# Kernel tuning notes

Measured on AMD Instinct MI355X. Metric: run time of the kernel, lower is better.

Reference implementation:

```python
import jax, jax.numpy as jnp
import numpy as np

N, T, CIN, H, L, NC = 64, 150, 150, 1024, 3, 60
EPS = 1e-5


def setup_inputs() -> dict:
    key = jax.random.key(0)
    ks = jax.random.split(key, 12)
    s = 0.05
    return {
        "x": jax.random.normal(ks[0], (N, T, CIN), jnp.float32),
        "bn_gamma": jnp.ones((CIN,), jnp.float32),
        "bn_beta": jnp.zeros((CIN,), jnp.float32),
        "w_ih0": jax.random.normal(ks[1], (2, 3 * H, CIN), jnp.float32) * s,
        "w_hh0": jax.random.normal(ks[2], (2, 3 * H, H), jnp.float32) * s,
        "b_ih0": jax.random.normal(ks[3], (2, 3 * H), jnp.float32) * s,
        "b_hh0": jax.random.normal(ks[4], (2, 3 * H), jnp.float32) * s,
        "w_ih": jax.random.normal(ks[5], (L - 1, 2, 3 * H, 2 * H), jnp.float32) * s,
        "w_hh": jax.random.normal(ks[6], (L - 1, 2, 3 * H, H), jnp.float32) * s,
        "b_ih": jax.random.normal(ks[7], (L - 1, 2, 3 * H), jnp.float32) * s,
        "b_hh": jax.random.normal(ks[8], (L - 1, 2, 3 * H), jnp.float32) * s,
        "fc_w": jax.random.normal(ks[9], (NC, 2 * H), jnp.float32) * s,
        "fc_b": jax.random.normal(ks[10], (NC,), jnp.float32) * s,
    }


def _bigru_layer(x, w_ih, w_hh, b_ih, b_hh):
    # x: [T, N, I]. Faithful to the source's per-timestep loop: BOTH directions
    # scan forward in time (the 'reverse' direction never sees a reversed seq,
    # since the original feeds length-1 slices while carrying hidden state).
    # Precompute input projections for the whole sequence: [T, 2, N, 3H]
    gi = jnp.einsum('tni,dgi->tdng', x, w_ih) + b_ih[None, :, None, :]

    def step(h, gi_t):
        # h: [2, N, H], gi_t: [2, N, 3H]
        gh = jnp.einsum('dnh,dgh->dng', h, w_hh) + b_hh[:, None, :]
        r = jax.nn.sigmoid(gi_t[..., :H] + gh[..., :H])
        z = jax.nn.sigmoid(gi_t[..., H:2 * H] + gh[..., H:2 * H])
        n = jnp.tanh(gi_t[..., 2 * H:] + r * gh[..., 2 * H:])
        h_new = (1.0 - z) * n + z * h
        out = jnp.concatenate([h_new[0], h_new[1]], axis=-1)  # [N, 2H]
        return h_new, out

    h0 = jnp.zeros((2, x.shape[1], H), x.dtype)
    _, outs = jax.lax.scan(step, h0, gi)
    return outs  # [T, N, 2H]


def reference(x, bn_gamma, bn_beta, w_ih0, w_hh0, b_ih0, b_hh0,
              w_ih, w_hh, b_ih, b_hh, fc_w, fc_b):
    # BatchNorm1d over channels, train mode: batch stats over (N, T), biased var.
    mean = x.mean(axis=(0, 1))
    var = x.var(axis=(0, 1))
    xn = (x - mean) * jax.lax.rsqrt(var + EPS) * bn_gamma + bn_beta

    h = jnp.transpose(xn, (1, 0, 2))  # [T, N, CIN]
    h = _bigru_layer(h, w_ih0, w_hh0, b_ih0, b_hh0)
    for l in range(L - 1):  # small fixed layer loop
        h = _bigru_layer(h, w_ih[l], w_hh[l], b_ih[l], b_hh[l])

    # seq_len == T for every sample, so the gathered hidden is the last step.
    last = h[-1]  # [N, 2H]
    return last @ fc_w.T + fc_b  # [N, num_class]
```

## Files before the change

### kernel.cpp

```cpp
#include <hip/hip_runtime.h>
#include <math.h>

#define NB   64
#define TT   150
#define CIN  150
#define HH   1024
#define G3   3072
#define NCOL 6144
#define KP0  160
#define RT   9600
#define NC   60
#define NSLOT 151
#define SLOT_STRIDE 66560

using bf16x8 = __attribute__((ext_vector_type(8))) __bf16;
using f32x4  = __attribute__((ext_vector_type(4))) float;

static __device__ __forceinline__ unsigned short f2bf(float f){
  unsigned int x = __builtin_bit_cast(unsigned int, f);
  x += 0x7fffu + ((x >> 16) & 1u);
  return (unsigned short)(x >> 16);
}
static __device__ __forceinline__ float bf2f(unsigned short u){
  unsigned int x = ((unsigned int)u) << 16;
  return __builtin_bit_cast(float, x);
}
static __device__ __forceinline__ float sigmoidf(float x){
  return 1.0f / (1.0f + expf(-x));
}

static __device__ __forceinline__ void gload16(const void* g, void* l){
  __builtin_amdgcn_global_load_lds(
      (const __attribute__((address_space(1))) void*)g,
      (__attribute__((address_space(3))) void*)l, 16, 0, 0);
}

__global__ void bn_stats(const float* __restrict__ x, const float* __restrict__ gamma,
                         const float* __restrict__ beta, float* __restrict__ ss){
  const int c = blockIdx.x;
  float s = 0.f, s2 = 0.f;
  for (int i = threadIdx.x; i < RT; i += 256){
    float v = x[(size_t)i * CIN + c];
    s += v; s2 += v * v;
  }
  __shared__ float sh1[256], sh2[256];
  sh1[threadIdx.x] = s; sh2[threadIdx.x] = s2;
  __syncthreads();
  for (int st = 128; st > 0; st >>= 1){
    if ((int)threadIdx.x < st){
      sh1[threadIdx.x] += sh1[threadIdx.x + st];
      sh2[threadIdx.x] += sh2[threadIdx.x + st];
    }
    __syncthreads();
  }
  if (threadIdx.x == 0){
    float mean = sh1[0] * (1.f / RT);
    float var  = sh2[0] * (1.f / RT) - mean * mean;
    float sc   = rsqrtf(var + 1e-5f) * gamma[c];
    ss[c]       = sc;
    ss[CIN + c] = beta[c] - mean * sc;
  }
}

__global__ void bn_apply(const float* __restrict__ x, const float* __restrict__ ss,
                         unsigned short* __restrict__ xn){
  int idx = blockIdx.x * 256 + threadIdx.x;
  if (idx >= RT * KP0) return;
  int r = idx / KP0, c = idx - r * KP0;
  int t = r >> 6, n = r & 63;
  float v = 0.f;
  if (c < CIN) v = x[((size_t)n * TT + t) * CIN + c] * ss[c] + ss[CIN + c];
  xn[idx] = f2bf(v);
}

__global__ void cast_bf(const float* __restrict__ s, unsigned short* __restrict__ d, int n){
  for (int i = blockIdx.x * 256 + threadIdx.x; i < n; i += gridDim.x * 256)
    d[i] = f2bf(s[i]);
}

__global__ void cast_pad_w0(const float* __restrict__ w, unsigned short* __restrict__ d){
  int idx = blockIdx.x * 256 + threadIdx.x;
  if (idx >= NCOL * KP0) return;
  int row = idx / KP0, c = idx - row * KP0;
  d[idx] = (c < CIN) ? f2bf(w[(size_t)row * CIN + c]) : (unsigned short)0;
}

__global__ void zero16(uint4* p, int n){
  int i = blockIdx.x * 256 + threadIdx.x;
  if (i < n) p[i] = make_uint4(0u, 0u, 0u, 0u);
}

__global__ void guard_k(float* out){ out[0] = -12345.0f; }

__global__ __launch_bounds__(256) void gemm_tile(
    const unsigned short* __restrict__ A, const unsigned short* __restrict__ B,
    const float* __restrict__ bias, unsigned short* __restrict__ C, int K)
{
  const int r0 = blockIdx.x * 128;
  const int c0 = blockIdx.y * 128;
  const int tid = threadIdx.x;
  const int wid = tid >> 6;
  const int l   = tid & 63;
  const int lr  = l & 15;
  const int lk  = (l >> 4) * 8;
  const int wm  = wid >> 1;
  const int wn  = wid & 1;

  __shared__ unsigned short As[128 * 32];
  __shared__ unsigned short Bs[128 * 32];

  const int c1   = wid * 64 + l;
  const int rowS = c1 >> 2;
  const int ccS  = c1 & 3;

  f32x4 acc[4][4];
#pragma unroll
  for (int i = 0; i < 4; ++i)
#pragma unroll
    for (int j = 0; j < 4; ++j) acc[i][j] = f32x4{0,0,0,0};

  const unsigned short* Ag0 = A + (size_t)(r0 + rowS) * K + ccS * 8;
  const unsigned short* Ag1 = A + (size_t)(r0 + 64 + rowS) * K + ccS * 8;
  const unsigned short* Bg0 = B + (size_t)(c0 + rowS) * K + ccS * 8;
  const unsigned short* Bg1 = B + (size_t)(c0 + 64 + rowS) * K + ccS * 8;
  unsigned short* As0 = As + wid * 512;
  unsigned short* As1 = As + 2048 + wid * 512;
  unsigned short* Bs0 = Bs + wid * 512;
  unsigned short* Bs1 = Bs + 2048 + wid * 512;

  for (int k0 = 0; k0 < K; k0 += 32){
    gload16(Ag0 + k0, As0);
    gload16(Ag1 + k0, As1);
    gload16(Bg0 + k0, Bs0);
    gload16(Bg1 + k0, Bs1);
    __syncthreads();

    bf16x8 af[4], bfr[4];
#pragma unroll
    for (int mt = 0; mt < 4; ++mt)
      af[mt] = *(const bf16x8*)(As + (wm * 64 + mt * 16 + lr) * 32 + lk);
#pragma unroll
    for (int nt = 0; nt < 4; ++nt)
      bfr[nt] = *(const bf16x8*)(Bs + (wn * 64 + nt * 16 + lr) * 32 + lk);
#pragma unroll
    for (int mt = 0; mt < 4; ++mt)
#pragma unroll
      for (int nt = 0; nt < 4; ++nt)
        acc[mt][nt] = __builtin_amdgcn_mfma_f32_16x16x32_bf16(af[mt], bfr[nt], acc[mt][nt], 0, 0, 0);
    __syncthreads();
  }

  const int rb = (l >> 4) * 4;
#pragma unroll
  for (int mt = 0; mt < 4; ++mt){
#pragma unroll
    for (int nt = 0; nt < 4; ++nt){
      const int col = c0 + wn * 64 + nt * 16 + lr;
      const float bv = bias[col];
#pragma unroll
      for (int reg = 0; reg < 4; ++reg){
        const int row = r0 + wm * 64 + mt * 16 + rb + reg;
        C[(size_t)row * NCOL + col] = f2bf(acc[mt][nt][reg] + bv);
      }
    }
  }
}

__global__ __launch_bounds__(512, 1) void gru_layer(
    const unsigned short* __restrict__ whh,
    const float* __restrict__ bhh,
    const unsigned short* __restrict__ gi,
    unsigned short* __restrict__ outb,
    float* __restrict__ hfinal,
    unsigned short* __restrict__ hbig,
    int* __restrict__ flags, int wout)
{
  const int d  = blockIdx.x >> 6;
  const int jt = blockIdx.x & 63;
  const int j0 = jt * 16;
  const int tid = threadIdx.x;
  const int w  = tid >> 6;
  const int wq = w & 3;
  const int kh = w >> 2;
  const int l  = tid & 63;
  const int lr = l & 15;
  const int hi = l >> 4;

  __shared__ unsigned char wlds[98304];
  __shared__ f32x4 red[3][256];

  {
    const unsigned short* wsrc = whh + (size_t)d * (G3 * HH);
    for (int c = tid; c < 6144; c += 512){
      int g   = c >> 11;
      int rem = c & 2047;
      int r   = rem >> 7;
      int kc  = rem & 127;
      uint4 v = *(const uint4*)(wsrc + (size_t)(g * HH + j0 + r) * HH + kc * 8);
      int kcs = (kc & ~7) | ((kc + r) & 7);
      *(uint4*)(wlds + g * 32768 + r * 2048 + kcs * 16) = v;
    }
  }
  __syncthreads();

  float4 br4 = make_float4(0, 0, 0, 0), bz4 = br4, bn4 = br4;
  if (w < 4){
    br4 = *(const float4*)(bhh + d * G3 +          j0 + hi * 4);
    bz4 = *(const float4*)(bhh + d * G3 + HH +     j0 + hi * 4);
    bn4 = *(const float4*)(bhh + d * G3 + 2 * HH + j0 + hi * 4);
  }

  const int n    = wq * 16 + lr;
  const int jcol = j0 + hi * 4;

  unsigned short* dirbase = hbig + (size_t)d * NSLOT * SLOT_STRIDE;
  int* ctr = &flags[d * 64];

  float hold[4] = {0.f, 0.f, 0.f, 0.f};

  for (int t = 0; t < TT; ++t){
    const unsigned short* hprev = dirbase + (size_t)t * SLOT_STRIDE;
    unsigned short*       hnext = dirbase + (size_t)(t + 1) * SLOT_STRIDE;

    ushort4 gr4, gz4, gn4;
    if (w < 4){
      size_t gbase = (size_t)(t * NB + n) * NCOL + (size_t)d * G3 + jcol;
      gr4 = *(const ushort4*)(gi + gbase);
      gz4 = *(const ushort4*)(gi + gbase + HH);
      gn4 = *(const ushort4*)(gi + gbase + 2 * HH);
    }

    if (t){
      if (tid == 0){
        const int tgt = 64 * t;
        int cap = 0;
        while (__hip_atomic_load(ctr, __ATOMIC_RELAXED, __HIP_MEMORY_SCOPE_AGENT) < tgt){
          if (++cap > 20000000) break;
          __builtin_amdgcn_s_sleep(1);
        }
      }
      __syncthreads();
    }

    f32x4 ar = {0,0,0,0}, az = {0,0,0,0}, an = {0,0,0,0};
    const unsigned short* hrow = hprev + (size_t)n * HH + kh * 512 + hi * 8;

    bf16x8 ha[8], hb2[8];
#pragma unroll
    for (int i = 0; i < 8; ++i) ha[i] = *(const bf16x8*)(hrow + i * 32);

#pragma unroll
    for (int half = 0; half < 2; ++half){
      if (half == 0){
#pragma unroll
        for (int i = 0; i < 8; ++i)
          hb2[i] = *(const bf16x8*)(hrow + 256 + i * 32);
      }
#pragma unroll
      for (int i = 0; i < 8; ++i){
        const int it  = half * 8 + i;
        const int kc  = kh * 64 + it * 4 + hi;
        const int kcs = (kc & ~7) | ((kc + lr) & 7);
        const int off = lr * 2048 + kcs * 16;
        bf16x8 a_r = *(const bf16x8*)(wlds +          off);
        bf16x8 a_z = *(const bf16x8*)(wlds + 32768 +  off);
        bf16x8 a_n = *(const bf16x8*)(wlds + 65536 +  off);
        ar = __builtin_amdgcn_mfma_f32_16x16x32_bf16(a_r, ha[i], ar, 0, 0, 0);
        az = __builtin_amdgcn_mfma_f32_16x16x32_bf16(a_z, ha[i], az, 0, 0, 0);
        an = __builtin_amdgcn_mfma_f32_16x16x32_bf16(a_n, ha[i], an, 0, 0, 0);
      }
      if (half == 0){
#pragma unroll
        for (int i = 0; i < 8; ++i) ha[i] = hb2[i];
      }
    }

    __syncthreads();
    if (w >= 4){
      red[0][wq * 64 + l] = ar;
      red[1][wq * 64 + l] = az;
      red[2][wq * 64 + l] = an;
    }
    __syncthreads();

    if (w < 4){
      ar += red[0][wq * 64 + l];
      az += red[1][wq * 64 + l];
      an += red[2][wq * 64 + l];

      ushort4 hb_;
      const float* br = (const float*)&br4;
      const float* bz = (const float*)&bz4;
      const float* bn_ = (const float*)&bn4;
      const unsigned short* g_r = (const unsigned short*)&gr4;
      const unsigned short* g_z = (const unsigned short*)&gz4;
      const unsigned short* g_n = (const unsigned short*)&gn4;
#pragma unroll
      for (int reg = 0; reg < 4; ++reg){
        float r  = sigmoidf(bf2f(g_r[reg]) + ar[reg] + br[reg]);
        float z  = sigmoidf(bf2f(g_z[reg]) + az[reg] + bz[reg]);
        float nn = tanhf(bf2f(g_n[reg]) + r * (an[reg] + bn_[reg]));
        hold[reg] = (1.f - z) * nn + z * hold[reg];
      }
      hb_.x = f2bf(hold[0]); hb_.y = f2bf(hold[1]);
      hb_.z = f2bf(hold[2]); hb_.w = f2bf(hold[3]);
      __hip_atomic_store((unsigned long long*)(hnext + (size_t)n * HH + jcol),
                         __builtin_bit_cast(unsigned long long, hb_),
                         __ATOMIC_RELAXED, __HIP_MEMORY_SCOPE_AGENT);
      if (wout)
        *(ushort4*)(outb + (size_t)(t * NB + n) * (2 * HH) + (size_t)d * HH + jcol) = hb_;
      if (t == TT - 1)
        *(float4*)(hfinal + (size_t)(d * NB + n) * HH + jcol) =
            make_float4(hold[0], hold[1], hold[2], hold[3]);
    }

    __syncthreads();
    if (tid == 0)
      __hip_atomic_fetch_add(ctr, 1, __ATOMIC_RELEASE, __HIP_MEMORY_SCOPE_AGENT);
  }
}

__global__ void fc_kernel(const float* __restrict__ hf, const float* __restrict__ fw,
                          const float* __restrict__ fb, float* __restrict__ out){
  int b = blockIdx.x;
  int n = b / NC, c = b - n * NC;
  int l = threadIdx.x;
  float s = 0.f;
  for (int k = l; k < 2 * HH; k += 64){
    float hv = (k < HH) ? hf[(size_t)n * HH + k]
                        : hf[(size_t)(NB + n) * HH + (k - HH)];
    s += hv * fw[(size_t)c * (2 * HH) + k];
  }
#pragma unroll
  for (int off = 32; off > 0; off >>= 1) s += __shfl_down(s, off);
  if (l == 0) out[n * NC + c] = s + fb[c];
}

extern "C" void kernel_launch(void* const* d_in, const int* in_sizes, int n_in,
                              void* d_out, int out_size, void* d_ws, size_t ws_size,
                              hipStream_t stream)
{
  const float* x      = (const float*)d_in[0];
  const float* gamma  = (const float*)d_in[1];
  const float* beta   = (const float*)d_in[2];
  const float* w_ih0  = (const float*)d_in[3];
  const float* w_hh0  = (const float*)d_in[4];
  const float* b_ih0  = (const float*)d_in[5];
  const float* b_hh0  = (const float*)d_in[6];
  const float* w_ih   = (const float*)d_in[7];
  const float* w_hh   = (const float*)d_in[8];
  const float* b_ih   = (const float*)d_in[9];
  const float* b_hh   = (const float*)d_in[10];
  const float* fc_w   = (const float*)d_in[11];
  const float* fc_b   = (const float*)d_in[12];
  float* out = (float*)d_out;

  char* ws = (char*)d_ws;
  size_t off = 0;
  auto alloc = [&](size_t bytes)->void*{
    void* p = ws + off; off += (bytes + 255) & ~(size_t)255; return p;
  };
  unsigned short* whh_bf = (unsigned short*)alloc((size_t)3 * 2 * G3 * HH * 2);
  unsigned short* w0_bf  = (unsigned short*)alloc((size_t)NCOL * KP0 * 2);
  unsigned short* wih_bf = (unsigned short*)alloc((size_t)2 * NCOL * 2 * HH * 2);
  unsigned short* xn_bf  = (unsigned short*)alloc((size_t)RT * KP0 * 2);
  unsigned short* gi_bf  = (unsigned short*)alloc((size_t)RT * NCOL * 2);
  unsigned short* out0   = (unsigned short*)alloc((size_t)RT * 2 * HH * 2);
  unsigned short* out1   = (unsigned short*)alloc((size_t)RT * 2 * HH * 2);
  float* hfinal = (float*)alloc((size_t)2 * NB * HH * 4);
  unsigned short* hbig = (unsigned short*)alloc((size_t)2 * NSLOT * SLOT_STRIDE * 2);
  float* ss = (float*)alloc(2048);
  int* flags = (int*)alloc(1024);

  if (off > ws_size){ guard_k<<<1, 1, 0, stream>>>(out); return; }

  bn_stats<<<CIN, 256, 0, stream>>>(x, gamma, beta, ss);
  bn_apply<<<(RT * KP0 + 255) / 256, 256, 0, stream>>>(x, ss, xn_bf);
  cast_pad_w0<<<(NCOL * KP0 + 255) / 256, 256, 0, stream>>>(w_ih0, w0_bf);
  cast_bf<<<4096, 256, 0, stream>>>(w_hh0, whh_bf, 2 * G3 * HH);
  cast_bf<<<4096, 256, 0, stream>>>(w_hh,  whh_bf + (size_t)2 * G3 * HH, 2 * 2 * G3 * HH);
  cast_bf<<<4096, 256, 0, stream>>>(w_ih,  wih_bf, 2 * NCOL * 2 * HH);

  zero16<<<32, 256, 0, stream>>>((uint4*)hbig, NB * HH * 2 / 16);
  zero16<<<32, 256, 0, stream>>>((uint4*)(hbig + (size_t)NSLOT * SLOT_STRIDE),
                                 NB * HH * 2 / 16);

  for (int lyr = 0; lyr < 3; ++lyr){
    if (lyr == 0){
      gemm_tile<<<dim3(RT / 128, NCOL / 128), 256, 0, stream>>>(xn_bf, w0_bf, b_ih0, gi_bf, KP0);
    } else {
      const unsigned short* Ain = (lyr == 1) ? out0 : out1;
      gemm_tile<<<dim3(RT / 128, NCOL / 128), 256, 0, stream>>>(
          Ain, wih_bf + (size_t)(lyr - 1) * NCOL * 2 * HH,
          b_ih + (size_t)(lyr - 1) * NCOL, gi_bf, 2 * HH);
    }
    zero16<<<1, 32, 0, stream>>>((uint4*)flags, 512 / 16);

    const unsigned short* whh_l = whh_bf + (size_t)lyr * 2 * G3 * HH;
    const float* bhh_l = (lyr == 0) ? b_hh0 : (b_hh + (size_t)(lyr - 1) * NCOL);
    unsigned short* outb = (lyr == 0) ? out0 : out1;
    int wout = (lyr < 2) ? 1 : 0;
    gru_layer<<<128, 512, 0, stream>>>(whh_l, bhh_l, gi_bf, outb,
                                       hfinal, hbig, flags, wout);
  }
  fc_kernel<<<NB * NC, 64, 0, stream>>>(hfinal, fc_w, fc_b, out);
}
```

Measured before the change: 5.444 ms.

## Keep recurrent weights in registers and split K four ways across waves

The W_hh tile is now held in VGPRs per wave (24 bf16x8 fragments) instead of staged in LDS. The work split moves from 4 batch groups by 2 K-halves to 2 batch groups by 4 K-quarters, with each wave computing two 16-row batch tiles. This removes the per-step LDS weight reads, and each weight fragment now feeds two MFMAs. In exchange the register footprint is much larger and the cross-wave reduction through LDS triples in size, with only a quarter of the waves doing the gate math.

```diff
diff --git a/kernel.cpp b/kernel.cpp
--- a/kernel.cpp
+++ b/kernel.cpp
@@ -180,54 +180,54 @@
   const int j0 = jt * 16;
   const int tid = threadIdx.x;
   const int w  = tid >> 6;
-  const int wq = w & 3;
-  const int kh = w >> 2;
+  const int kq = w & 3;
+  const int nh = w >> 2;
   const int l  = tid & 63;
   const int lr = l & 15;
   const int hi = l >> 4;
 
-  __shared__ unsigned char wlds[98304];
-  __shared__ f32x4 red[3][256];
-
-  {
-    const unsigned short* wsrc = whh + (size_t)d * (G3 * HH);
-    for (int c = tid; c < 6144; c += 512){
-      int g   = c >> 11;
-      int rem = c & 2047;
-      int r   = rem >> 7;
-      int kc  = rem & 127;
-      uint4 v = *(const uint4*)(wsrc + (size_t)(g * HH + j0 + r) * HH + kc * 8);
-      int kcs = (kc & ~7) | ((kc + r) & 7);
-      *(uint4*)(wlds + g * 32768 + r * 2048 + kcs * 16) = v;
-    }
-  }
-  __syncthreads();
+  __shared__ f32x4 red4[2304];
+
+  bf16x8 wf[3][8];
+#pragma unroll
+  for (int g = 0; g < 3; ++g){
+    const unsigned short* wbase = whh + (size_t)d * (G3 * HH)
+        + (size_t)(g * HH + j0 + lr) * HH + kq * 256 + hi * 8;
+#pragma unroll
+    for (int ks = 0; ks < 8; ++ks)
+      wf[g][ks] = *(const bf16x8*)(wbase + ks * 32);
+  }
 
   float4 br4 = make_float4(0, 0, 0, 0), bz4 = br4, bn4 = br4;
-  if (w < 4){
+  if (kq == 0){
     br4 = *(const float4*)(bhh + d * G3 +          j0 + hi * 4);
     bz4 = *(const float4*)(bhh + d * G3 + HH +     j0 + hi * 4);
     bn4 = *(const float4*)(bhh + d * G3 + 2 * HH + j0 + hi * 4);
   }
-
-  const int n    = wq * 16 + lr;
   const int jcol = j0 + hi * 4;
+  const int n0 = nh * 32 + lr;
+  const int n1 = nh * 32 + 16 + lr;
 
   unsigned short* dirbase = hbig + (size_t)d * NSLOT * SLOT_STRIDE;
   int* ctr = &flags[d * 64];
 
-  float hold[4] = {0.f, 0.f, 0.f, 0.f};
+  float hold0[4] = {0.f, 0.f, 0.f, 0.f};
+  float hold1[4] = {0.f, 0.f, 0.f, 0.f};
 
   for (int t = 0; t < TT; ++t){
     const unsigned short* hprev = dirbase + (size_t)t * SLOT_STRIDE;
     unsigned short*       hnext = dirbase + (size_t)(t + 1) * SLOT_STRIDE;
 
-    ushort4 gr4, gz4, gn4;
-    if (w < 4){
-      size_t gbase = (size_t)(t * NB + n) * NCOL + (size_t)d * G3 + jcol;
-      gr4 = *(const ushort4*)(gi + gbase);
-      gz4 = *(const ushort4*)(gi + gbase + HH);
-      gn4 = *(const ushort4*)(gi + gbase + 2 * HH);
+    ushort4 gr0, gz0, gn0, gr1, gz1, gn1;
+    if (kq == 0){
+      size_t gb0 = (size_t)(t * NB + n0) * NCOL + (size_t)d * G3 + jcol;
+      size_t gb1 = (size_t)(t * NB + n1) * NCOL + (size_t)d * G3 + jcol;
+      gr0 = *(const ushort4*)(gi + gb0);
+      gz0 = *(const ushort4*)(gi + gb0 + HH);
+      gn0 = *(const ushort4*)(gi + gb0 + 2 * HH);
+      gr1 = *(const ushort4*)(gi + gb1);
+      gz1 = *(const ushort4*)(gi + gb1 + HH);
+      gn1 = *(const ushort4*)(gi + gb1 + 2 * HH);
     }
 
     if (t){
@@ -242,76 +242,97 @@
       __syncthreads();
     }
 
-    f32x4 ar = {0,0,0,0}, az = {0,0,0,0}, an = {0,0,0,0};
-    const unsigned short* hrow = hprev + (size_t)n * HH + kh * 512 + hi * 8;
-
-    bf16x8 ha[8], hb2[8];
-#pragma unroll
-    for (int i = 0; i < 8; ++i) ha[i] = *(const bf16x8*)(hrow + i * 32);
-
-#pragma unroll
-    for (int half = 0; half < 2; ++half){
-      if (half == 0){
-#pragma unroll
-        for (int i = 0; i < 8; ++i)
-          hb2[i] = *(const bf16x8*)(hrow + 256 + i * 32);
-      }
-#pragma unroll
-      for (int i = 0; i < 8; ++i){
-        const int it  = half * 8 + i;
-        const int kc  = kh * 64 + it * 4 + hi;
-        const int kcs = (kc & ~7) | ((kc + lr) & 7);
-        const int off = lr * 2048 + kcs * 16;
-        bf16x8 a_r = *(const bf16x8*)(wlds +          off);
-        bf16x8 a_z = *(const bf16x8*)(wlds + 32768 +  off);
-        bf16x8 a_n = *(const bf16x8*)(wlds + 65536 +  off);
-        ar = __builtin_amdgcn_mfma_f32_16x16x32_bf16(a_r, ha[i], ar, 0, 0, 0);
-        az = __builtin_amdgcn_mfma_f32_16x16x32_bf16(a_z, ha[i], az, 0, 0, 0);
-        an = __builtin_amdgcn_mfma_f32_16x16x32_bf16(a_n, ha[i], an, 0, 0, 0);
-      }
-      if (half == 0){
-#pragma unroll
-        for (int i = 0; i < 8; ++i) ha[i] = hb2[i];
-      }
-    }
-
-    __syncthreads();
-    if (w >= 4){
-      red[0][wq * 64 + l] = ar;
-      red[1][wq * 64 + l] = az;
-      red[2][wq * 64 + l] = an;
-    }
-    __syncthreads();
-
-    if (w < 4){
-      ar += red[0][wq * 64 + l];
-      az += red[1][wq * 64 + l];
-      an += red[2][wq * 64 + l];
-
-      ushort4 hb_;
+    const unsigned short* hb0p = hprev + (size_t)n0 * HH + kq * 256 + hi * 8;
+    const unsigned short* hb1p = hprev + (size_t)n1 * HH + kq * 256 + hi * 8;
+    bf16x8 hf0[8], hf1[8];
+#pragma unroll
+    for (int ks = 0; ks < 8; ++ks){
+      hf0[ks] = *(const bf16x8*)(hb0p + ks * 32);
+      hf1[ks] = *(const bf16x8*)(hb1p + ks * 32);
+    }
+
+    f32x4 acc[3][2];
+#pragma unroll
+    for (int g = 0; g < 3; ++g){ acc[g][0] = f32x4{0,0,0,0}; acc[g][1] = f32x4{0,0,0,0}; }
+#pragma unroll
+    for (int ks = 0; ks < 8; ++ks){
+#pragma unroll
+      for (int g = 0; g < 3; ++g){
+        acc[g][0] = __builtin_amdgcn_mfma_f32_16x16x32_bf16(wf[g][ks], hf0[ks], acc[g][0], 0, 0, 0);
+        acc[g][1] = __builtin_amdgcn_mfma_f32_16x16x32_bf16(wf[g][ks], hf1[ks], acc[g][1], 0, 0, 0);
+      }
+    }
+
+    __syncthreads();
+    if (kq > 0){
+      const int src = (kq - 1) * 2 + nh;
+#pragma unroll
+      for (int g = 0; g < 3; ++g){
+        red4[(src * 6 + g * 2 + 0) * 64 + l] = acc[g][0];
+        red4[(src * 6 + g * 2 + 1) * 64 + l] = acc[g][1];
+      }
+    }
+    __syncthreads();
+
+    if (kq == 0){
+#pragma unroll
+      for (int kqp = 1; kqp < 4; ++kqp){
+        const int src = (kqp - 1) * 2 + nh;
+#pragma unroll
+        for (int g = 0; g < 3; ++g){
+          acc[g][0] += red4[(src * 6 + g * 2 + 0) * 64 + l];
+          acc[g][1] += red4[(src * 6 + g * 2 + 1) * 64 + l];
+        }
+      }
+
       const float* br = (const float*)&br4;
       const float* bz = (const float*)&bz4;
       const float* bn_ = (const float*)&bn4;
-      const unsigned short* g_r = (const unsigned short*)&gr4;
-      const unsigned short* g_z = (const unsigned short*)&gz4;
-      const unsigned short* g_n = (const unsigned short*)&gn4;
-#pragma unroll
-      for (int reg = 0; reg < 4; ++reg){
-        float r  = sigmoidf(bf2f(g_r[reg]) + ar[reg] + br[reg]);
-        float z  = sigmoidf(bf2f(g_z[reg]) + az[reg] + bz[reg]);
-        float nn = tanhf(bf2f(g_n[reg]) + r * (an[reg] + bn_[reg]));
-        hold[reg] = (1.f - z) * nn + z * hold[reg];
-      }
-      hb_.x = f2bf(hold[0]); hb_.y = f2bf(hold[1]);
-      hb_.z = f2bf(hold[2]); hb_.w = f2bf(hold[3]);
-      __hip_atomic_store((unsigned long long*)(hnext + (size_t)n * HH + jcol),
-                         __builtin_bit_cast(unsigned long long, hb_),
+      ushort4 hbv0, hbv1;
+      {
+        const unsigned short* g_r = (const unsigned short*)&gr0;
+        const unsigned short* g_z = (const unsigned short*)&gz0;
+        const unsigned short* g_n = (const unsigned short*)&gn0;
+#pragma unroll
+        for (int reg = 0; reg < 4; ++reg){
+          float r  = sigmoidf(bf2f(g_r[reg]) + acc[0][0][reg] + br[reg]);
+          float z  = sigmoidf(bf2f(g_z[reg]) + acc[1][0][reg] + bz[reg]);
+          float nn = tanhf(bf2f(g_n[reg]) + r * (acc[2][0][reg] + bn_[reg]));
+          hold0[reg] = (1.f - z) * nn + z * hold0[reg];
+        }
+        hbv0.x = f2bf(hold0[0]); hbv0.y = f2bf(hold0[1]);
+        hbv0.z = f2bf(hold0[2]); hbv0.w = f2bf(hold0[3]);
+      }
+      {
+        const unsigned short* g_r = (const unsigned short*)&gr1;
+        const unsigned short* g_z = (const unsigned short*)&gz1;
+        const unsigned short* g_n = (const unsigned short*)&gn1;
+#pragma unroll
+        for (int reg = 0; reg < 4; ++reg){
+          float r  = sigmoidf(bf2f(g_r[reg]) + acc[0][1][reg] + br[reg]);
+          float z  = sigmoidf(bf2f(g_z[reg]) + acc[1][1][reg] + bz[reg]);
+          float nn = tanhf(bf2f(g_n[reg]) + r * (acc[2][1][reg] + bn_[reg]));
+          hold1[reg] = (1.f - z) * nn + z * hold1[reg];
+        }
+        hbv1.x = f2bf(hold1[0]); hbv1.y = f2bf(hold1[1]);
+        hbv1.z = f2bf(hold1[2]); hbv1.w = f2bf(hold1[3]);
+      }
+      __hip_atomic_store((unsigned long long*)(hnext + (size_t)n0 * HH + jcol),
+                         __builtin_bit_cast(unsigned long long, hbv0),
                          __ATOMIC_RELAXED, __HIP_MEMORY_SCOPE_AGENT);
-      if (wout)
-        *(ushort4*)(outb + (size_t)(t * NB + n) * (2 * HH) + (size_t)d * HH + jcol) = hb_;
-      if (t == TT - 1)
-        *(float4*)(hfinal + (size_t)(d * NB + n) * HH + jcol) =
-            make_float4(hold[0], hold[1], hold[2], hold[3]);
+      __hip_atomic_store((unsigned long long*)(hnext + (size_t)n1 * HH + jcol),
+                         __builtin_bit_cast(unsigned long long, hbv1),
+                         __ATOMIC_RELAXED, __HIP_MEMORY_SCOPE_AGENT);
+      if (wout){
+        *(ushort4*)(outb + (size_t)(t * NB + n0) * (2 * HH) + (size_t)d * HH + jcol) = hbv0;
+        *(ushort4*)(outb + (size_t)(t * NB + n1) * (2 * HH) + (size_t)d * HH + jcol) = hbv1;
+      }
+      if (t == TT - 1){
+        *(float4*)(hfinal + (size_t)(d * NB + n0) * HH + jcol) =
+            make_float4(hold0[0], hold0[1], hold0[2], hold0[3]);
+        *(float4*)(hfinal + (size_t)(d * NB + n1) * HH + jcol) =
+            make_float4(hold1[0], hold1[1], hold1[2], hold1[3]);
+      }
     }
 
     __syncthreads();
```

Result: slower. 5.943 ms (+9.2%).

## Split per-step grid barrier into per-K-half counters with wave-level waiting

Applied to the files above, without the earlier changes.

The single per-direction step counter, polled by one thread and followed by block-wide barriers, is replaced by two counters, one per K-half of the hidden state. Waves 0 and 7 poll the counter for their own half and publish readiness through an LDS flag that the other waves spin on. Each reducing wave now bumps its counter directly, and the cross-wave reduction buffer is double-buffered by step parity, which removes two of the three __syncthreads per timestep. The aim is to shorten the serial per-step latency of the recurrent loop by letting each K-half begin as soon as its inputs are ready. In exchange it adds more spinning waves and relies on subtler memory ordering between the relaxed LDS flag and the global hidden-state reads.

```diff
diff --git a/kernel.cpp b/kernel.cpp
--- a/kernel.cpp
+++ b/kernel.cpp
@@ -187,7 +187,10 @@
   const int hi = l >> 4;
 
   __shared__ unsigned char wlds[98304];
-  __shared__ f32x4 red[3][256];
+  __shared__ f32x4 red[2][3][256];
+  __shared__ int go[2];
+
+  if (tid == 0){ go[0] = 0; go[1] = 0; }
 
   {
     const unsigned short* wsrc = whh + (size_t)d * (G3 * HH);
@@ -214,7 +217,10 @@
   const int jcol = j0 + hi * 4;
 
   unsigned short* dirbase = hbig + (size_t)d * NSLOT * SLOT_STRIDE;
-  int* ctr = &flags[d * 64];
+  int* ctrA = &flags[d * 128];
+  int* ctrB = &flags[d * 128 + 64];
+  int* myctr = (kh == 0) ? ctrA : ctrB;
+  int* bumpc = (jt < 32) ? ctrA : ctrB;
 
   float hold[4] = {0.f, 0.f, 0.f, 0.f};
 
@@ -231,15 +237,25 @@
     }
 
     if (t){
-      if (tid == 0){
-        const int tgt = 64 * t;
-        int cap = 0;
-        while (__hip_atomic_load(ctr, __ATOMIC_RELAXED, __HIP_MEMORY_SCOPE_AGENT) < tgt){
-          if (++cap > 20000000) break;
-          __builtin_amdgcn_s_sleep(1);
+      if (w == 0 || w == 7){
+        if (l == 0){
+          const int tgt = 128 * t;
+          int cap = 0;
+          while (__hip_atomic_load(myctr, __ATOMIC_RELAXED, __HIP_MEMORY_SCOPE_AGENT) < tgt){
+            if (++cap > 20000000) break;
+            __builtin_amdgcn_s_sleep(2);
+          }
+          __hip_atomic_store(&go[kh], t, __ATOMIC_RELAXED, __HIP_MEMORY_SCOPE_WORKGROUP);
         }
-      }
-      __syncthreads();
+      } else {
+        if (l == 0){
+          int cap = 0;
+          while (__hip_atomic_load(&go[kh], __ATOMIC_RELAXED, __HIP_MEMORY_SCOPE_WORKGROUP) < t){
+            if (++cap > 40000000) break;
+            __builtin_amdgcn_s_sleep(1);
+          }
+        }
+      }
     }
 
     f32x4 ar = {0,0,0,0}, az = {0,0,0,0}, an = {0,0,0,0};
@@ -275,18 +291,18 @@
       }
     }
 
+    const int par = t & 1;
+    if (kh == 1){
+      red[par][0][wq * 64 + l] = ar;
+      red[par][1][wq * 64 + l] = az;
+      red[par][2][wq * 64 + l] = an;
+    }
     __syncthreads();
-    if (w >= 4){
-      red[0][wq * 64 + l] = ar;
-      red[1][wq * 64 + l] = az;
-      red[2][wq * 64 + l] = an;
-    }
-    __syncthreads();
 
     if (w < 4){
-      ar += red[0][wq * 64 + l];
-      az += red[1][wq * 64 + l];
-      an += red[2][wq * 64 + l];
+      ar += red[par][0][wq * 64 + l];
+      az += red[par][1][wq * 64 + l];
+      an += red[par][2][wq * 64 + l];
 
       ushort4 hb_;
       const float* br = (const float*)&br4;
@@ -312,11 +328,9 @@
       if (t == TT - 1)
         *(float4*)(hfinal + (size_t)(d * NB + n) * HH + jcol) =
             make_float4(hold[0], hold[1], hold[2], hold[3]);
-    }
-
-    __syncthreads();
-    if (tid == 0)
-      __hip_atomic_fetch_add(ctr, 1, __ATOMIC_RELEASE, __HIP_MEMORY_SCOPE_AGENT);
+      if (l == 0)
+        __hip_atomic_fetch_add(bumpc, 1, __ATOMIC_RELEASE, __HIP_MEMORY_SCOPE_AGENT);
+    }
   }
 }
 
@@ -394,7 +408,7 @@
           Ain, wih_bf + (size_t)(lyr - 1) * NCOL * 2 * HH,
           b_ih + (size_t)(lyr - 1) * NCOL, gi_bf, 2 * HH);
     }
-    zero16<<<1, 32, 0, stream>>>((uint4*)flags, 512 / 16);
+    zero16<<<1, 64, 0, stream>>>((uint4*)flags, 1024 / 16);
 
     const unsigned short* whh_l = whh_bf + (size_t)lyr * 2 * G3 * HH;
     const float* bhh_l = (lyr == 0) ? b_hh0 : (b_hh + (size_t)(lyr - 1) * NCOL);
```

Result: slower. 10.12 ms (+85.9%).
